# Optimization experiments

Hardware: AMD Instinct MI355X
Metric: run time of the kernel (lower is better)

The kernel has to match this reference:

```python
import jax, jax.numpy as jnp
import numpy as np

B, L, DIM = 2, 2048, 1024
H, DH, W = 16, 64, 256  # heads, head_dim, window_size
ROPE_BASE = 10000.0


def _rope(x):
    # x: [b, l, h, d] -> rotate consecutive pairs (torch view_as_complex semantics)
    l, d = x.shape[1], x.shape[3]
    freqs = 1.0 / (ROPE_BASE ** (jnp.arange(0, d, 2, dtype=jnp.float32) / d))  # [d/2]
    ang = jnp.arange(l, dtype=jnp.float32)[:, None] * freqs[None, :]           # [l, d/2]
    cos = jnp.cos(ang)[None, :, None, :].astype(x.dtype)
    sin = jnp.sin(ang)[None, :, None, :].astype(x.dtype)
    xe, xo = x[..., 0::2], x[..., 1::2]
    ye = xe * cos - xo * sin
    yo = xe * sin + xo * cos
    return jnp.stack([ye, yo], axis=-1).reshape(x.shape)


def setup_inputs() -> dict:
    key = jax.random.key(0)
    ks = jax.random.split(key, 7)
    sh = (B, L, DIM)
    return {
        "q": jax.random.normal(ks[0], sh, jnp.float32),
        "k": jax.random.normal(ks[1], sh, jnp.float32),
        "v": jax.random.normal(ks[2], sh, jnp.float32),
        "wq": jax.random.normal(ks[3], (H * DH, DIM), jnp.float32) * 0.02,
        "wk": jax.random.normal(ks[4], (H * DH, DIM), jnp.float32) * 0.02,
        "wv": jax.random.normal(ks[5], (H * DH, DIM), jnp.float32) * 0.02,
        "wo": jax.random.normal(ks[6], (DIM, H * DH), jnp.float32) * 0.02,
    }


def reference(q, k, v, wq, wk, wv, wo):
    b, l, _ = q.shape
    qh = (q @ wq.T).reshape(b, l, H, DH)
    kh = (k @ wk.T).reshape(b, l, H, DH)
    vh = (v @ wv.T).reshape(b, l, H, DH).transpose(0, 2, 1, 3)  # [b,h,l,d]
    qh = _rope(qh).transpose(0, 2, 1, 3)                        # [b,h,l,d]
    kh = _rope(kh).transpose(0, 2, 1, 3)
    scores = jnp.einsum('bhqd,bhkd->bhqk', qh, kh) * (DH ** -0.5)
    i = jnp.arange(l)[:, None]
    j = jnp.arange(l)[None, :]
    window_mask = (j <= i) & (j >= i - W)  # keys in [i-W, i], matches the loop
    scores = jnp.where(window_mask, scores, -1e30)
    probs = jax.nn.softmax(scores, axis=-1)
    out = jnp.einsum('bhqk,bhkd->bhqd', probs, vh)
    out = out.transpose(0, 2, 1, 3).reshape(b, l, H * DH)
    return out @ wo.T
```

## Files before the change

kernel.cpp:

```cpp
#include <hip/hip_runtime.h>
#include <stdint.h>

#define B_    2
#define L_    2048
#define DIM_  1024
#define H_    16
#define DH_   64
#define WWIN  256

typedef __attribute__((ext_vector_type(4))) float f32x4;
typedef __attribute__((ext_vector_type(8))) short bf16x8;

__device__ __forceinline__ unsigned short f2bf(float x) {
  union { float f; unsigned u; } c; c.f = x;
  unsigned r = c.u + 0x7fffu + ((c.u >> 16) & 1u);
  return (unsigned short)(r >> 16);
}

struct CastArgs {
  const float* src[7];
  unsigned short* dst[7];
  int n[7];
};
__global__ __launch_bounds__(256) void cast_bf16_kernel(CastArgs a) {
  int arr = blockIdx.y;
  int i = (blockIdx.x * 256 + threadIdx.x) * 4;
  if (i >= a.n[arr]) return;
  float4 v = *(const float4*)(a.src[arr] + i);
  ushort4 o;
  o.x = f2bf(v.x); o.y = f2bf(v.y); o.z = f2bf(v.z); o.w = f2bf(v.w);
  *(ushort4*)(a.dst[arr] + i) = o;
}

#define BM 128
#define BN 64
#define BK 64

__device__ __forceinline__ void gld_lds16(const void* g, void* l) {
  __builtin_amdgcn_global_load_lds(
      (const __attribute__((address_space(1))) void*)g,
      (__attribute__((address_space(3))) void*)l, 16, 0, 0);
}

__device__ __forceinline__ void gemm_core_1024(
    const unsigned short* __restrict__ A, const unsigned short* __restrict__ Bt,
    unsigned short* As, unsigned short* Bs, f32x4 (&acc)[2][4],
    int m0, int n0) {
  const int tid = threadIdx.x;
  const int wave = tid >> 6, lane = tid & 63;
  const int quad = lane >> 4, l16 = lane & 15;
  const int srow = tid >> 3, sc = tid & 7;

  auto stage = [&](int k0, int buf) {
    unsigned short* Ad = As + buf * 8192;
    unsigned short* Bd = Bs + buf * 4096;
    #pragma unroll
    for (int rd = 0; rd < 4; ++rd) {
      int row = rd * 32 + srow;
      int cs = sc ^ (row & 7);
      gld_lds16(A + (size_t)(m0 + row) * 1024 + k0 + cs * 8, Ad + row * BK + sc * 8);
    }
    #pragma unroll
    for (int rd = 0; rd < 2; ++rd) {
      int row = rd * 32 + srow;
      int cs = sc ^ (row & 7);
      gld_lds16(Bt + (size_t)(n0 + row) * 1024 + k0 + cs * 8, Bd + row * BK + sc * 8);
    }
  };

  stage(0, 0);
  for (int k = 0; k < 16; ++k) {
    const int cur = k & 1;
    __syncthreads();
    if (k < 15) stage((k + 1) * BK, cur ^ 1);
    const unsigned short* Ac = As + cur * 8192;
    const unsigned short* Bc = Bs + cur * 4096;
    #pragma unroll
    for (int ks = 0; ks < 2; ++ks) {
      bf16x8 af[2], bfr[4];
      #pragma unroll
      for (int i = 0; i < 2; ++i) {
        int row = wave * 32 + i * 16 + l16;
        int ch = (ks * 4 + quad) ^ (row & 7);
        af[i] = *(const bf16x8*)(Ac + row * BK + ch * 8);
      }
      #pragma unroll
      for (int j = 0; j < 4; ++j) {
        int row = j * 16 + l16;
        int ch = (ks * 4 + quad) ^ (row & 7);
        bfr[j] = *(const bf16x8*)(Bc + row * BK + ch * 8);
      }
      #pragma unroll
      for (int i = 0; i < 2; ++i)
        #pragma unroll
        for (int j = 0; j < 4; ++j)
          acc[i][j] = __builtin_amdgcn_mfma_f32_16x16x32_bf16(af[i], bfr[j], acc[i][j], 0, 0, 0);
    }
  }
}

struct ProjArgs {
  const unsigned short* A[3];
  const unsigned short* Bt[3];
  unsigned short* C[3];
};
__global__ __launch_bounds__(256) void gemm_proj_kernel(ProjArgs pa) {
  __shared__ unsigned short SH[24576];
  unsigned short* As = SH;
  unsigned short* Bs = SH + 16384;

  const int bflat = blockIdx.x;
  const int xcd = bflat & 7, s = bflat >> 3;
  const int nblk = s & 15;
  const int mz = xcd * 12 + (s >> 4);
  const int z = mz >> 5;
  const int mblk = mz & 31;
  const int m0 = mblk * BM, n0 = nblk * BN;

  f32x4 acc[2][4] = {};
  gemm_core_1024(pa.A[z], pa.Bt[z], As, Bs, acc, m0, n0);

  const int tid = threadIdx.x;
  const int lane = tid & 63, wave = tid >> 6;
  const int quad = lane >> 4, l16 = lane & 15;

  if (z < 2) {
    float frev[4];
    #pragma unroll
    for (int j = 0; j < 4; ++j) {
      int d = j * 16 + l16;
      frev[j] = exp2f(-(float)(d >> 1) * 0.41524101186092029f) * 0.15915494309189535f;
    }
    unsigned short* C = pa.C[z];
    const int h = nblk;
    const bool even = (l16 & 1) == 0;
    #pragma unroll
    for (int i = 0; i < 2; ++i)
      #pragma unroll
      for (int r = 0; r < 4; ++r) {
        int m = m0 + wave * 32 + i * 16 + quad * 4 + r;
        int b = m >> 11, l = m & (L_ - 1);
        float lf = (float)l;
        #pragma unroll
        for (int j = 0; j < 4; ++j) {
          int d = j * 16 + l16;
          float v = acc[i][j][r];
          float p = __shfl_xor(v, 1);
          float a = lf * frev[j];
          float t = a - floorf(a);
          float sn = __builtin_amdgcn_sinf(t);
          float cs = __builtin_amdgcn_cosf(t);
          float o = even ? (v * cs - p * sn) : (p * sn + v * cs);
          C[(((size_t)b * H_ + h) * L_ + l) * DH_ + d] = f2bf(o);
        }
      }
  } else {
    __syncthreads();
    unsigned short* T = SH + wave * 2304;
    #pragma unroll
    for (int i = 0; i < 2; ++i)
      #pragma unroll
      for (int j = 0; j < 4; ++j) {
        int nw = j * 16 + l16;
        int hm = i * 4 + quad;
        uint2 pk;
        pk.x = (unsigned)f2bf(acc[i][j][0]) | ((unsigned)f2bf(acc[i][j][1]) << 16);
        pk.y = (unsigned)f2bf(acc[i][j][2]) | ((unsigned)f2bf(acc[i][j][3]) << 16);
        *(uint2*)(T + nw * 36 + hm * 4) = pk;
      }
    asm volatile("s_waitcnt lgkmcnt(0)" ::: "memory");
    int h = nblk;
    int d = lane;
    int b = m0 >> 11;
    int lbase = (m0 & (L_ - 1)) + wave * 32;
    unsigned short* C = pa.C[2];
    size_t rowbase = (((size_t)b * H_ + h) * DH_ + d) * L_ + lbase;
    #pragma unroll
    for (int t = 0; t < 4; ++t) {
      uint2 lo = *(uint2*)(T + lane * 36 + t * 8);
      uint2 hi = *(uint2*)(T + lane * 36 + t * 8 + 4);
      uint4 o = {lo.x, lo.y, hi.x, hi.y};
      *(uint4*)(C + rowbase + t * 8) = o;
    }
  }
}

__global__ __launch_bounds__(256) void gemm_out_kernel(
    const unsigned short* __restrict__ A, const unsigned short* __restrict__ Bt,
    float* __restrict__ C) {
  __shared__ unsigned short SH[24576];
  unsigned short* As = SH;
  unsigned short* Bs = SH + 16384;

  const int bflat = blockIdx.x;
  const int xcd = bflat & 7, s = bflat >> 3;
  const int nblk = s & 15;
  const int mblk = xcd * 4 + (s >> 4);
  const int m0 = mblk * BM, n0 = nblk * BN;

  f32x4 acc[2][4] = {};
  gemm_core_1024(A, Bt, As, Bs, acc, m0, n0);

  const int lane = threadIdx.x & 63, wave = threadIdx.x >> 6;
  const int quad = lane >> 4, l16 = lane & 15;
  #pragma unroll
  for (int i = 0; i < 2; ++i)
    #pragma unroll
    for (int j = 0; j < 4; ++j)
      #pragma unroll
      for (int r = 0; r < 4; ++r) {
        int m = m0 + wave * 32 + i * 16 + quad * 4 + r;
        int n = n0 + j * 16 + l16;
        C[(size_t)m * DIM_ + n] = acc[i][j][r];
      }
}

#define NCH 17
__global__ __launch_bounds__(64) void attn_kernel(
    const unsigned short* __restrict__ Qh,
    const unsigned short* __restrict__ Kh,
    const unsigned short* __restrict__ Vt,
    unsigned short* __restrict__ O) {
  __shared__ unsigned short Ps[16 * 296];
  const int lane = threadIdx.x;
  const int quad = lane >> 4, l16 = lane & 15;

  const int bflat = blockIdx.x;
  const int xcd = bflat & 7, s = bflat >> 3;
  const int qt = s >> 2;
  const int bh = xcd * 4 + (s & 3);

  const int q0 = qt * 16;
  const int kwin0 = q0 - WWIN;

  const unsigned short* Kbase = Kh + (size_t)bh * L_ * DH_;
  const unsigned short* Vbase = Vt + (size_t)bh * DH_ * L_;

  bf16x8 qf0, qf1;
  {
    const unsigned short* qrow = Qh + ((size_t)bh * L_ + q0 + l16) * DH_;
    qf0 = *(const bf16x8*)(qrow + quad * 8);
    qf1 = *(const bf16x8*)(qrow + 32 + quad * 8);
  }

  f32x4 S[NCH] = {};
  #pragma unroll
  for (int cc = 0; cc < NCH; ++cc) {
    int key = kwin0 + cc * 16 + l16;
    key = key < 0 ? 0 : key;
    const unsigned short* kr = Kbase + (size_t)key * DH_;
    bf16x8 kf0 = *(const bf16x8*)(kr + quad * 8);
    bf16x8 kf1 = *(const bf16x8*)(kr + 32 + quad * 8);
    S[cc] = __builtin_amdgcn_mfma_f32_16x16x32_bf16(qf0, kf0, S[cc], 0, 0, 0);
    S[cc] = __builtin_amdgcn_mfma_f32_16x16x32_bf16(qf1, kf1, S[cc], 0, 0, 0);
  }

  float inv_l[4];
  #pragma unroll
  for (int r = 0; r < 4; ++r) {
    int i = q0 + quad * 4 + r;
    float mx = -1e30f;
    #pragma unroll
    for (int c = 0; c < NCH; ++c) {
      int key = kwin0 + c * 16 + l16;
      bool valid = (key >= 0) && (key <= i) && (key >= i - WWIN);
      float v = valid ? S[c][r] * 0.125f : -1e30f;
      S[c][r] = v;
      mx = fmaxf(mx, v);
    }
    mx = fmaxf(mx, __shfl_xor(mx, 1));
    mx = fmaxf(mx, __shfl_xor(mx, 2));
    mx = fmaxf(mx, __shfl_xor(mx, 4));
    mx = fmaxf(mx, __shfl_xor(mx, 8));
    float sum = 0.f;
    #pragma unroll
    for (int c = 0; c < NCH; ++c) {
      float e = __expf(S[c][r] - mx);
      S[c][r] = e;
      sum += e;
    }
    sum += __shfl_xor(sum, 1);
    sum += __shfl_xor(sum, 2);
    sum += __shfl_xor(sum, 4);
    sum += __shfl_xor(sum, 8);
    inv_l[r] = 1.0f / sum;
  }

  #pragma unroll
  for (int cc = 0; cc < NCH; ++cc)
    #pragma unroll
    for (int r = 0; r < 4; ++r)
      Ps[(quad * 4 + r) * 296 + cc * 16 + l16] = f2bf(S[cc][r] * inv_l[r]);
  #pragma unroll
  for (int r = 0; r < 4; ++r)
    Ps[(quad * 4 + r) * 296 + 272 + l16] = 0;
  asm volatile("s_waitcnt lgkmcnt(0)" ::: "memory");

  f32x4 Oacc[4] = {};
  #pragma unroll
  for (int g = 0; g < 9; ++g) {
    bf16x8 pf = *(const bf16x8*)(&Ps[l16 * 296 + g * 32 + quad * 8]);
    int kk = kwin0 + g * 32 + quad * 8;
    kk = kk < 0 ? 0 : kk;
    kk = kk > (L_ - 8) ? (L_ - 8) : kk;
    #pragma unroll
    for (int t = 0; t < 4; ++t) {
      bf16x8 vf = *(const bf16x8*)(Vbase + (size_t)(t * 16 + l16) * L_ + kk);
      Oacc[t] = __builtin_amdgcn_mfma_f32_16x16x32_bf16(pf, vf, Oacc[t], 0, 0, 0);
    }
  }

  int b = bh >> 4, h = bh & 15;
  #pragma unroll
  for (int t = 0; t < 4; ++t)
    #pragma unroll
    for (int r = 0; r < 4; ++r) {
      int l = q0 + quad * 4 + r;
      int col = h * DH_ + t * 16 + l16;
      O[((size_t)b * L_ + l) * (H_ * DH_) + col] = f2bf(Oacc[t][r]);
    }
}

extern "C" void kernel_launch(void* const* d_in, const int* in_sizes, int n_in,
                              void* d_out, int out_size, void* d_ws, size_t ws_size,
                              hipStream_t stream) {
  const float* q  = (const float*)d_in[0];
  const float* k  = (const float*)d_in[1];
  const float* v  = (const float*)d_in[2];
  const float* wq = (const float*)d_in[3];
  const float* wk = (const float*)d_in[4];
  const float* wv = (const float*)d_in[5];
  const float* wo = (const float*)d_in[6];

  const size_t SA = (size_t)B_ * L_ * DIM_;
  const size_t SW = (size_t)DIM_ * DIM_;
  unsigned short* w   = (unsigned short*)d_ws;
  unsigned short* qb  = w; w += SA;
  unsigned short* kb  = w; w += SA;
  unsigned short* vb  = w; w += SA;
  unsigned short* wqb = w; w += SW;
  unsigned short* wkb = w; w += SW;
  unsigned short* wvb = w; w += SW;
  unsigned short* wob = w; w += SW;
  unsigned short* qh  = w; w += SA;
  unsigned short* kh  = w; w += SA;
  unsigned short* vt  = w; w += SA;
  unsigned short* Ob  = w; w += SA;

  CastArgs ca;
  ca.src[0] = q;  ca.dst[0] = qb;  ca.n[0] = (int)SA;
  ca.src[1] = k;  ca.dst[1] = kb;  ca.n[1] = (int)SA;
  ca.src[2] = v;  ca.dst[2] = vb;  ca.n[2] = (int)SA;
  ca.src[3] = wq; ca.dst[3] = wqb; ca.n[3] = (int)SW;
  ca.src[4] = wk; ca.dst[4] = wkb; ca.n[4] = (int)SW;
  ca.src[5] = wv; ca.dst[5] = wvb; ca.n[5] = (int)SW;
  ca.src[6] = wo; ca.dst[6] = wob; ca.n[6] = (int)SW;
  cast_bf16_kernel<<<dim3(SA / (256 * 4), 7), 256, 0, stream>>>(ca);

  ProjArgs pa;
  pa.A[0] = qb; pa.Bt[0] = wqb; pa.C[0] = qh;
  pa.A[1] = kb; pa.Bt[1] = wkb; pa.C[1] = kh;
  pa.A[2] = vb; pa.Bt[2] = wvb; pa.C[2] = vt;
  gemm_proj_kernel<<<dim3(16 * 32 * 3), 256, 0, stream>>>(pa);

  attn_kernel<<<dim3(128 * 32), 64, 0, stream>>>(qh, kh, vt, Ob);
  gemm_out_kernel<<<dim3(16 * 32), 256, 0, stream>>>(Ob, wob, (float*)d_out);
}
```

Baseline: 197.6 us.

## Load GEMM A operand directly to registers and pack four attention tiles per block

The shared GEMM core stops staging the A tile through LDS. Each wave now loads its own A rows straight from global memory into double-buffered registers, and only B goes through LDS, which cuts LDS footprint and LDS read traffic. Separately, the attention kernel now runs four 16-query tiles per 256-thread block, one per wave, each with its own LDS P buffer, so the launch uses a quarter as many blocks. The risks are uncoalesced direct global loads for A and higher register pressure from the fully unrolled k loop.

```diff
diff --git a/kernel.cpp b/kernel.cpp
--- a/kernel.cpp
+++ b/kernel.cpp
@@ -44,22 +44,17 @@
 
 __device__ __forceinline__ void gemm_core_1024(
     const unsigned short* __restrict__ A, const unsigned short* __restrict__ Bt,
-    unsigned short* As, unsigned short* Bs, f32x4 (&acc)[2][4],
-    int m0, int n0) {
+    unsigned short* Bs, f32x4 (&acc)[2][4], int m0, int n0) {
   const int tid = threadIdx.x;
   const int wave = tid >> 6, lane = tid & 63;
   const int quad = lane >> 4, l16 = lane & 15;
   const int srow = tid >> 3, sc = tid & 7;
 
-  auto stage = [&](int k0, int buf) {
-    unsigned short* Ad = As + buf * 8192;
+  const unsigned short* Arow0 = A + (size_t)(m0 + wave * 32 + l16) * 1024 + quad * 8;
+  const unsigned short* Arow1 = Arow0 + (size_t)16 * 1024;
+
+  auto stageB = [&](int k0, int buf) {
     unsigned short* Bd = Bs + buf * 4096;
-    #pragma unroll
-    for (int rd = 0; rd < 4; ++rd) {
-      int row = rd * 32 + srow;
-      int cs = sc ^ (row & 7);
-      gld_lds16(A + (size_t)(m0 + row) * 1024 + k0 + cs * 8, Ad + row * BK + sc * 8);
-    }
     #pragma unroll
     for (int rd = 0; rd < 2; ++rd) {
       int row = rd * 32 + srow;
@@ -68,22 +63,28 @@
     }
   };
 
-  stage(0, 0);
+  bf16x8 af[2][2][2];
+  auto loadA = [&](int k0, int buf) {
+    af[buf][0][0] = *(const bf16x8*)(Arow0 + k0);
+    af[buf][0][1] = *(const bf16x8*)(Arow0 + k0 + 32);
+    af[buf][1][0] = *(const bf16x8*)(Arow1 + k0);
+    af[buf][1][1] = *(const bf16x8*)(Arow1 + k0 + 32);
+  };
+
+  stageB(0, 0);
+  loadA(0, 0);
+  #pragma unroll
   for (int k = 0; k < 16; ++k) {
     const int cur = k & 1;
     __syncthreads();
-    if (k < 15) stage((k + 1) * BK, cur ^ 1);
-    const unsigned short* Ac = As + cur * 8192;
+    if (k < 15) {
+      stageB((k + 1) * BK, cur ^ 1);
+      loadA((k + 1) * BK, cur ^ 1);
+    }
     const unsigned short* Bc = Bs + cur * 4096;
     #pragma unroll
     for (int ks = 0; ks < 2; ++ks) {
-      bf16x8 af[2], bfr[4];
-      #pragma unroll
-      for (int i = 0; i < 2; ++i) {
-        int row = wave * 32 + i * 16 + l16;
-        int ch = (ks * 4 + quad) ^ (row & 7);
-        af[i] = *(const bf16x8*)(Ac + row * BK + ch * 8);
-      }
+      bf16x8 bfr[4];
       #pragma unroll
       for (int j = 0; j < 4; ++j) {
         int row = j * 16 + l16;
@@ -94,7 +95,7 @@
       for (int i = 0; i < 2; ++i)
         #pragma unroll
         for (int j = 0; j < 4; ++j)
-          acc[i][j] = __builtin_amdgcn_mfma_f32_16x16x32_bf16(af[i], bfr[j], acc[i][j], 0, 0, 0);
+          acc[i][j] = __builtin_amdgcn_mfma_f32_16x16x32_bf16(af[cur][i][ks], bfr[j], acc[i][j], 0, 0, 0);
     }
   }
 }
@@ -105,9 +106,8 @@
   unsigned short* C[3];
 };
 __global__ __launch_bounds__(256) void gemm_proj_kernel(ProjArgs pa) {
-  __shared__ unsigned short SH[24576];
-  unsigned short* As = SH;
-  unsigned short* Bs = SH + 16384;
+  __shared__ unsigned short SH[9216];
+  unsigned short* Bs = SH;
 
   const int bflat = blockIdx.x;
   const int xcd = bflat & 7, s = bflat >> 3;
@@ -118,7 +118,7 @@
   const int m0 = mblk * BM, n0 = nblk * BN;
 
   f32x4 acc[2][4] = {};
-  gemm_core_1024(pa.A[z], pa.Bt[z], As, Bs, acc, m0, n0);
+  gemm_core_1024(pa.A[z], pa.Bt[z], Bs, acc, m0, n0);
 
   const int tid = threadIdx.x;
   const int lane = tid & 63, wave = tid >> 6;
@@ -188,9 +188,8 @@
 __global__ __launch_bounds__(256) void gemm_out_kernel(
     const unsigned short* __restrict__ A, const unsigned short* __restrict__ Bt,
     float* __restrict__ C) {
-  __shared__ unsigned short SH[24576];
-  unsigned short* As = SH;
-  unsigned short* Bs = SH + 16384;
+  __shared__ unsigned short SH[8192];
+  unsigned short* Bs = SH;
 
   const int bflat = blockIdx.x;
   const int xcd = bflat & 7, s = bflat >> 3;
@@ -199,7 +198,7 @@
   const int m0 = mblk * BM, n0 = nblk * BN;
 
   f32x4 acc[2][4] = {};
-  gemm_core_1024(A, Bt, As, Bs, acc, m0, n0);
+  gemm_core_1024(A, Bt, Bs, acc, m0, n0);
 
   const int lane = threadIdx.x & 63, wave = threadIdx.x >> 6;
   const int quad = lane >> 4, l16 = lane & 15;
@@ -216,25 +215,27 @@
 }
 
 #define NCH 17
-__global__ __launch_bounds__(64) void attn_kernel(
+__global__ __launch_bounds__(256) void attn_kernel(
     const unsigned short* __restrict__ Qh,
     const unsigned short* __restrict__ Kh,
     const unsigned short* __restrict__ Vt,
     unsigned short* __restrict__ O) {
-  __shared__ unsigned short Ps[16 * 296];
-  const int lane = threadIdx.x;
+  __shared__ unsigned short Ps[4][16 * 296];
+  const int tid = threadIdx.x;
+  const int wave = tid >> 6, lane = tid & 63;
   const int quad = lane >> 4, l16 = lane & 15;
 
   const int bflat = blockIdx.x;
   const int xcd = bflat & 7, s = bflat >> 3;
-  const int qt = s >> 2;
   const int bh = xcd * 4 + (s & 3);
+  const int qt = (s >> 2) * 4 + wave;
 
   const int q0 = qt * 16;
   const int kwin0 = q0 - WWIN;
 
   const unsigned short* Kbase = Kh + (size_t)bh * L_ * DH_;
   const unsigned short* Vbase = Vt + (size_t)bh * DH_ * L_;
+  unsigned short* pw = &Ps[wave][0];
 
   bf16x8 qf0, qf1;
   {
@@ -290,16 +291,16 @@
   for (int cc = 0; cc < NCH; ++cc)
     #pragma unroll
     for (int r = 0; r < 4; ++r)
-      Ps[(quad * 4 + r) * 296 + cc * 16 + l16] = f2bf(S[cc][r] * inv_l[r]);
+      pw[(quad * 4 + r) * 296 + cc * 16 + l16] = f2bf(S[cc][r] * inv_l[r]);
   #pragma unroll
   for (int r = 0; r < 4; ++r)
-    Ps[(quad * 4 + r) * 296 + 272 + l16] = 0;
+    pw[(quad * 4 + r) * 296 + 272 + l16] = 0;
   asm volatile("s_waitcnt lgkmcnt(0)" ::: "memory");
 
   f32x4 Oacc[4] = {};
   #pragma unroll
   for (int g = 0; g < 9; ++g) {
-    bf16x8 pf = *(const bf16x8*)(&Ps[l16 * 296 + g * 32 + quad * 8]);
+    bf16x8 pf = *(const bf16x8*)(&pw[l16 * 296 + g * 32 + quad * 8]);
     int kk = kwin0 + g * 32 + quad * 8;
     kk = kk < 0 ? 0 : kk;
     kk = kk > (L_ - 8) ? (L_ - 8) : kk;
@@ -363,6 +364,6 @@
   pa.A[2] = vb; pa.Bt[2] = wvb; pa.C[2] = vt;
   gemm_proj_kernel<<<dim3(16 * 32 * 3), 256, 0, stream>>>(pa);
 
-  attn_kernel<<<dim3(128 * 32), 64, 0, stream>>>(qh, kh, vt, Ob);
+  attn_kernel<<<dim3(32 * 32), 256, 0, stream>>>(qh, kh, vt, Ob);
   gemm_out_kernel<<<dim3(16 * 32), 256, 0, stream>>>(Ob, wob, (float*)d_out);
 }
```

After: 232.6 us. 1.18x slower.
